# Performance work log

Hardware: AMD Instinct MI355X
Metric: run time of the kernel (lower is better)

The kernel has to match this reference:

```python
import jax, jax.numpy as jnp
import numpy as np

B = 8192          # num_envs
OPT = 16          # num options
SHARED = 22       # shared_state_size (hardcoded in module)
UNIQ = 8          # unique_state_size (hardcoded in module)
MIN_DUR, MAX_DUR = 0.1, 0.5  # const.gait_net.valid_swing_duration_range


def _w(k, o, i):
    return jax.random.normal(k, (o, i), jnp.float32) * (1.0 / np.sqrt(i))


def setup_inputs() -> dict:
    key = jax.random.key(0)
    ks = jax.random.split(key, 20)
    obs = jax.random.normal(ks[0], (B, SHARED + OPT * UNIQ), jnp.float32)
    flag = jax.random.uniform(ks[1], (B, OPT)) < 0.25
    u = obs[:, SHARED:].reshape(B, OPT, UNIQ)
    u = u.at[:, :, 0].set(jnp.where(flag, 1.0, u[:, :, 0]))
    obs = jnp.concatenate([obs[:, :SHARED], u.reshape(B, OPT * UNIQ)], axis=1)
    return {
        "obs": obs,
        "sw1": _w(ks[2], 256, 22), "sb1": jnp.zeros((256,), jnp.float32),
        "sw2": _w(ks[3], 256, 256), "sb2": jnp.zeros((256,), jnp.float32),
        "uw1": _w(ks[4], 128, 8), "ub1": jnp.zeros((128,), jnp.float32),
        "uw2": _w(ks[5], 128, 128), "ub2": jnp.zeros((128,), jnp.float32),
        "no_op_embedding": jax.random.normal(ks[6], (128,), jnp.float32),
        "tw1": _w(ks[7], 512, 384), "tb1": jnp.zeros((512,), jnp.float32),
        "tw2": _w(ks[8], 256, 512), "tb2": jnp.zeros((256,), jnp.float32),
        "vw": _w(ks[9], 1, 256), "vb": jnp.zeros((1,), jnp.float32),
        "dw": _w(ks[10], 1, 256), "db": jnp.zeros((1,), jnp.float32),
    }


def reference(obs, sw1, sb1, sw2, sb2, uw1, ub1, uw2, ub2, no_op_embedding,
              tw1, tb1, tw2, tb2, vw, vb, dw, db):
    relu = jax.nn.relu
    shared = obs[:, :SHARED]                               # [B, 22]
    uniq = obs[:, SHARED:].reshape(B, OPT, UNIQ)           # [B, OPT, 8]
    # shared encoder (22 -> 256 -> 256, relu output)
    se = relu(relu(shared @ sw1.T + sb1) @ sw2.T + sb2)    # [B, 256]
    # unique encoder applied to all options at once (8 -> 128 -> 128)
    ue = relu(relu(uniq @ uw1.T + ub1) @ uw2.T + ub2)      # [B, OPT, 128]
    no_op = uniq[:, :, 0] == 1.0                           # [B, OPT]
    ue = jnp.where(no_op[..., None], no_op_embedding, ue)
    trunk_in = jnp.concatenate(
        [jnp.broadcast_to(se[:, None, :], (B, OPT, se.shape[-1])), ue], axis=-1)
    t = relu(relu(trunk_in @ tw1.T + tb1) @ tw2.T + tb2)   # [B, OPT, 256]
    logits = (t @ vw.T + vb).squeeze(-1)                   # [B, OPT]
    duration = jax.nn.sigmoid((t @ dw.T + db).squeeze(-1)) * (MAX_DUR - MIN_DUR) + MIN_DUR
    return logits, duration
```

## Files before the change

kernel.cpp:

```cpp
#include <hip/hip_runtime.h>
#include <stdint.h>


static constexpr int B_ = 8192;

typedef __attribute__((ext_vector_type(8))) short bf16x8;
typedef __attribute__((ext_vector_type(4))) float f32x4;

__device__ __forceinline__ float u2f(uint16_t u) {
    union { uint32_t i; float f; } c; c.i = (uint32_t)u << 16; return c.f;
}
__device__ __forceinline__ uint16_t f2u(float f) {
    union { float f; uint32_t i; } c; c.f = f;
    uint32_t x = c.i;
    return (uint16_t)((x + 0x7FFFu + ((x >> 16) & 1u)) >> 16);
}

static constexpr size_t WCSE   = 0;
static constexpr size_t WTW1SE = 4194304;
static constexpr size_t WTW1UE = WTW1SE + 131072;
static constexpr size_t WTW2   = WTW1UE + 65536;
static constexpr size_t WUW2   = WTW2 + 131072;
static constexpr size_t WSW2   = WUW2 + 16384;
static constexpr size_t WUW1B  = WSW2 + 65536;

__global__ __launch_bounds__(256) void k_conv(
    const float* __restrict__ tw1, const float* __restrict__ tw2,
    const float* __restrict__ uw2, const float* __restrict__ sw2,
    const float* __restrict__ uw1, uint16_t* __restrict__ ws)
{
    int i4 = blockIdx.x * 256 + threadIdx.x;
    if (i4 >= 102400) {
        int q = i4 - 102400;
        int n = q >> 3, k0 = (q & 7) * 4;
        ushort4 o = {0, 0, 0, 0};
        if (k0 < 8) {
            float4 v = *reinterpret_cast<const float4*>(uw1 + n * 8 + k0);
            o.x = f2u(v.x); o.y = f2u(v.y); o.z = f2u(v.z); o.w = f2u(v.w);
        }
        *reinterpret_cast<ushort4*>(ws + WUW1B + n * 32 + k0) = o;
        return;
    }
    const float* src; size_t dst;
    if (i4 < 32768) {
        int g = i4 * 4, n = g >> 8, k = g & 255;
        src = tw1 + (size_t)n * 384 + k;
        dst = WTW1SE + (size_t)g;
    } else if (i4 < 49152) {
        int q = i4 - 32768, n = q >> 5, w = q & 31;
        src = tw1 + (size_t)n * 384 + 256 + w * 4;
        dst = WTW1UE + (size_t)n * 128 + w * 4;
    } else if (i4 < 81920) {
        int q = (i4 - 49152) * 4;
        src = tw2 + q; dst = WTW2 + q;
    } else if (i4 < 86016) {
        int q = (i4 - 81920) * 4;
        src = uw2 + q; dst = WUW2 + q;
    } else {
        int q = (i4 - 86016) * 4;
        src = sw2 + q; dst = WSW2 + q;
    }
    float4 v = *reinterpret_cast<const float4*>(src);
    ushort4 o;
    o.x = f2u(v.x); o.y = f2u(v.y); o.z = f2u(v.z); o.w = f2u(v.w);
    *reinterpret_cast<ushort4*>(ws + dst) = o;
}

__global__ __launch_bounds__(512) void k_cse(
    const float* __restrict__ obs,
    const float* __restrict__ sw1, const float* __restrict__ sb1,
    const float* __restrict__ sb2, const float* __restrict__ tb1,
    uint16_t* __restrict__ ws)
{
    __shared__ float xs[16][24];
    __shared__ uint16_t h1s[16 * 264];
    __shared__ uint16_t seL[16 * 264];
    const int t = threadIdx.x;
    const int b0 = blockIdx.x * 16;
    const uint16_t* sw2b   = ws + WSW2;
    const uint16_t* tw1seb = ws + WTW1SE;

    if (t < 352) {
        int e = t / 22, c = t - e * 22;
        xs[e][c] = obs[(size_t)(b0 + e) * 150 + c];
    }
    __syncthreads();
    {
        const int n = t & 255;
        float w[22];
        #pragma unroll
        for (int k = 0; k < 22; ++k) w[k] = sw1[n * 22 + k];
        const float bias = sb1[n];
        #pragma unroll
        for (int ii = 0; ii < 8; ++ii) {
            int e = (t >> 8) * 8 + ii;
            float a = bias;
            #pragma unroll
            for (int k = 0; k < 22; ++k) a += w[k] * xs[e][k];
            h1s[e * 264 + n] = f2u(fmaxf(a, 0.f));
        }
    }
    __syncthreads();
    const int wv = t >> 6, lane = t & 63, quad = lane >> 4, l16 = lane & 15;
    {
        f32x4 acc[2];
        #pragma unroll
        for (int nt = 0; nt < 2; ++nt) {
            float bv = sb2[wv * 32 + nt * 16 + l16];
            acc[nt] = {bv, bv, bv, bv};
        }
        const uint16_t* bb = sw2b + (size_t)(wv * 32 + l16) * 256 + quad * 8;
        bf16x8 bc[2], bn[2];
        bc[0] = *reinterpret_cast<const bf16x8*>(bb);
        bc[1] = *reinterpret_cast<const bf16x8*>(bb + 4096);
        #pragma unroll
        for (int kk = 0; kk < 8; ++kk) {
            if (kk < 7) {
                bn[0] = *reinterpret_cast<const bf16x8*>(bb + (kk + 1) * 32);
                bn[1] = *reinterpret_cast<const bf16x8*>(bb + 4096 + (kk + 1) * 32);
            }
            bf16x8 af = *reinterpret_cast<const bf16x8*>(
                &h1s[l16 * 264 + kk * 32 + quad * 8]);
            #pragma unroll
            for (int nt = 0; nt < 2; ++nt)
                acc[nt] = __builtin_amdgcn_mfma_f32_16x16x32_bf16(
                    af, bc[nt], acc[nt], 0, 0, 0);
            bc[0] = bn[0]; bc[1] = bn[1];
        }
        #pragma unroll
        for (int nt = 0; nt < 2; ++nt)
            #pragma unroll
            for (int r = 0; r < 4; ++r)
                seL[(quad * 4 + r) * 264 + wv * 32 + nt * 16 + l16] =
                    f2u(fmaxf(acc[nt][r], 0.f));
    }
    __syncthreads();
    {
        f32x4 acc[4];
        #pragma unroll
        for (int nt = 0; nt < 4; ++nt) {
            float bv = tb1[wv * 64 + nt * 16 + l16];
            acc[nt] = {bv, bv, bv, bv};
        }
        const uint16_t* bb = tw1seb + (size_t)(wv * 64 + l16) * 256 + quad * 8;
        bf16x8 bc[4], bn[4];
        #pragma unroll
        for (int nt = 0; nt < 4; ++nt)
            bc[nt] = *reinterpret_cast<const bf16x8*>(bb + nt * 4096);
        #pragma unroll
        for (int kk = 0; kk < 8; ++kk) {
            if (kk < 7) {
                #pragma unroll
                for (int nt = 0; nt < 4; ++nt)
                    bn[nt] = *reinterpret_cast<const bf16x8*>(
                        bb + nt * 4096 + (kk + 1) * 32);
            }
            bf16x8 af = *reinterpret_cast<const bf16x8*>(
                &seL[l16 * 264 + kk * 32 + quad * 8]);
            #pragma unroll
            for (int nt = 0; nt < 4; ++nt)
                acc[nt] = __builtin_amdgcn_mfma_f32_16x16x32_bf16(
                    af, bc[nt], acc[nt], 0, 0, 0);
            #pragma unroll
            for (int nt = 0; nt < 4; ++nt) bc[nt] = bn[nt];
        }
        #pragma unroll
        for (int nt = 0; nt < 4; ++nt)
            #pragma unroll
            for (int r = 0; r < 4; ++r)
                ws[WCSE + (size_t)(b0 + quad * 4 + r) * 512 +
                   wv * 64 + nt * 16 + l16] = f2u(acc[nt][r]);
    }
}

static constexpr int UQB_OFF  = 0;
static constexpr int NOOP_OFF = 5120;
static constexpr int CSE_OFF  = 5376;
static constexpr int H1U_OFF  = 9472;
static constexpr int UET_OFF  = 26880;
static constexpr int H1T_OFF  = 44288;
static constexpr int SMEM_SZ  = 78080;

__global__ __launch_bounds__(512, 4) void k_main(
    const float* __restrict__ obs,
    const float* __restrict__ ub1,
    const float* __restrict__ ub2, const float* __restrict__ emb,
    const float* __restrict__ tb2,
    const float* __restrict__ vw,  const float* __restrict__ vb,
    const float* __restrict__ dw,  const float* __restrict__ db,
    const uint16_t* __restrict__ wsb,
    float* __restrict__ out)
{
    __shared__ __align__(16) char smem[SMEM_SZ];
    uint16_t* uqb   = (uint16_t*)(smem + UQB_OFF);
    float*    noopf = (float*)(smem + NOOP_OFF);
    uint16_t* cseL  = (uint16_t*)(smem + CSE_OFF);
    uint16_t* h1u   = (uint16_t*)(smem + H1U_OFF);
    uint16_t* uet   = (uint16_t*)(smem + UET_OFF);
    uint16_t* h1t   = (uint16_t*)(smem + H1T_OFF);
    uint16_t* t2    = h1t;

    const int t    = threadIdx.x;
    const int wv   = t >> 6;
    const int lane = t & 63;
    const int quad = lane >> 4;
    const int l16  = lane & 15;
    const int b0   = blockIdx.x * 4;

    const uint16_t* csep  = wsb + WCSE;
    const uint16_t* tw1ue = wsb + WTW1UE;
    const uint16_t* tw2b  = wsb + WTW2;
    const uint16_t* uw2b  = wsb + WUW2;
    const uint16_t* uw1b  = wsb + WUW1B;

    {
        int r = t >> 3, q = t & 7;
        int e = r >> 4, o = r & 15;
        ushort4 ov = {0, 0, 0, 0};
        if (q < 2) {
            const float2* sp = reinterpret_cast<const float2*>(
                &obs[(size_t)(b0 + e) * 150 + 22 + o * 8 + q * 4]);
            float2 a = sp[0], b = sp[1];
            ov.x = f2u(a.x); ov.y = f2u(a.y); ov.z = f2u(b.x); ov.w = f2u(b.y);
        }
        *reinterpret_cast<ushort4*>(&uqb[r * 40 + q * 4]) = ov;
        #pragma unroll
        for (int ii = 0; ii < 2; ++ii) {
            int i = t + ii * 512;
            int ee = i >> 8, cc = i & 255;
            ((uint32_t*)cseL)[ee * 256 + cc] =
                ((const uint32_t*)(csep + (size_t)(b0 + ee) * 512))[cc];
        }
        if (t < 64) {
            int ee = t >> 4, oo = t & 15;
            noopf[t] = (obs[(size_t)(b0 + ee) * 150 + 22 + oo * 8] == 1.0f) ? 1.0f : 0.0f;
        }
    }
    __syncthreads();

    {
        const int n = wv * 16 + l16;
        const float bv = ub1[n];
        f32x4 acc[4];
        #pragma unroll
        for (int mt = 0; mt < 4; ++mt) acc[mt] = {bv, bv, bv, bv};
        bf16x8 bf = *reinterpret_cast<const bf16x8*>(&uw1b[n * 32 + quad * 8]);
        #pragma unroll
        for (int mt = 0; mt < 4; ++mt) {
            bf16x8 af = *reinterpret_cast<const bf16x8*>(
                &uqb[(mt * 16 + l16) * 40 + quad * 8]);
            acc[mt] = __builtin_amdgcn_mfma_f32_16x16x32_bf16(af, bf, acc[mt], 0, 0, 0);
        }
        #pragma unroll
        for (int mt = 0; mt < 4; ++mt)
            #pragma unroll
            for (int r = 0; r < 4; ++r) {
                int row = mt * 16 + quad * 4 + r;
                h1u[row * 136 + n] = f2u(fmaxf(acc[mt][r], 0.f));
            }
    }
    __syncthreads();

    {
        const int n = wv * 16 + l16;
        const float bv = ub2[n];
        const float ev = emb[n];
        f32x4 acc[4];
        #pragma unroll
        for (int mt = 0; mt < 4; ++mt) acc[mt] = {bv, bv, bv, bv};
        #pragma unroll
        for (int kk = 0; kk < 4; ++kk) {
            bf16x8 bf = *reinterpret_cast<const bf16x8*>(
                &uw2b[(size_t)n * 128 + kk * 32 + quad * 8]);
            #pragma unroll
            for (int mt = 0; mt < 4; ++mt) {
                bf16x8 af = *reinterpret_cast<const bf16x8*>(
                    &h1u[(mt * 16 + l16) * 136 + kk * 32 + quad * 8]);
                acc[mt] = __builtin_amdgcn_mfma_f32_16x16x32_bf16(af, bf, acc[mt], 0, 0, 0);
            }
        }
        #pragma unroll
        for (int mt = 0; mt < 4; ++mt)
            #pragma unroll
            for (int r = 0; r < 4; ++r) {
                int row = mt * 16 + quad * 4 + r;
                float v = (noopf[row] != 0.0f) ? ev : fmaxf(acc[mt][r], 0.f);
                uet[row * 136 + n] = f2u(v);
            }
    }
    __syncthreads();

    f32x4 acc2[4][2];
    #pragma unroll
    for (int nt = 0; nt < 2; ++nt) {
        float bv = tb2[wv * 32 + nt * 16 + l16];
        #pragma unroll
        for (int mt = 0; mt < 4; ++mt) acc2[mt][nt] = {bv, bv, bv, bv};
    }

    #pragma unroll
    for (int nc = 0; nc < 2; ++nc) {
        {
            f32x4 acc1[4][2];
            #pragma unroll
            for (int nt = 0; nt < 2; ++nt) {
                int n = nc * 256 + wv * 32 + nt * 16 + l16;
                #pragma unroll
                for (int mt = 0; mt < 4; ++mt) {
                    float v = u2f(cseL[mt * 512 + n]);
                    acc1[mt][nt] = {v, v, v, v};
                }
            }
            const uint16_t* bb = tw1ue + (size_t)(nc * 256 + wv * 32 + l16) * 128
                                 + quad * 8;
            bf16x8 bc[2], bn[2];
            bc[0] = *reinterpret_cast<const bf16x8*>(bb);
            bc[1] = *reinterpret_cast<const bf16x8*>(bb + 2048);
            #pragma unroll
            for (int kk = 0; kk < 4; ++kk) {
                if (kk < 3) {
                    bn[0] = *reinterpret_cast<const bf16x8*>(bb + (kk + 1) * 32);
                    bn[1] = *reinterpret_cast<const bf16x8*>(bb + 2048 + (kk + 1) * 32);
                }
                bf16x8 af[4];
                #pragma unroll
                for (int mt = 0; mt < 4; ++mt)
                    af[mt] = *reinterpret_cast<const bf16x8*>(
                        &uet[(mt * 16 + l16) * 136 + kk * 32 + quad * 8]);
                #pragma unroll
                for (int mt = 0; mt < 4; ++mt)
                    #pragma unroll
                    for (int nt = 0; nt < 2; ++nt)
                        acc1[mt][nt] = __builtin_amdgcn_mfma_f32_16x16x32_bf16(
                            af[mt], bc[nt], acc1[mt][nt], 0, 0, 0);
                bc[0] = bn[0]; bc[1] = bn[1];
            }
            #pragma unroll
            for (int mt = 0; mt < 4; ++mt)
                #pragma unroll
                for (int nt = 0; nt < 2; ++nt)
                    #pragma unroll
                    for (int r = 0; r < 4; ++r) {
                        int row = mt * 16 + quad * 4 + r;
                        h1t[row * 264 + wv * 32 + nt * 16 + l16] =
                            f2u(fmaxf(acc1[mt][nt][r], 0.f));
                    }
        }
        __syncthreads();
        {
            const uint16_t* cb = tw2b + (size_t)(wv * 32 + l16) * 512 + nc * 256
                                 + quad * 8;
            bf16x8 cc[2], cn[2];
            cc[0] = *reinterpret_cast<const bf16x8*>(cb);
            cc[1] = *reinterpret_cast<const bf16x8*>(cb + 8192);
            #pragma unroll
            for (int k2 = 0; k2 < 8; ++k2) {
                if (k2 < 7) {
                    cn[0] = *reinterpret_cast<const bf16x8*>(cb + (k2 + 1) * 32);
                    cn[1] = *reinterpret_cast<const bf16x8*>(cb + 8192 + (k2 + 1) * 32);
                }
                bf16x8 af[4];
                #pragma unroll
                for (int mt = 0; mt < 4; ++mt)
                    af[mt] = *reinterpret_cast<const bf16x8*>(
                        &h1t[(mt * 16 + l16) * 264 + k2 * 32 + quad * 8]);
                #pragma unroll
                for (int mt = 0; mt < 4; ++mt)
                    #pragma unroll
                    for (int nt = 0; nt < 2; ++nt)
                        acc2[mt][nt] = __builtin_amdgcn_mfma_f32_16x16x32_bf16(
                            af[mt], cc[nt], acc2[mt][nt], 0, 0, 0);
                cc[0] = cn[0]; cc[1] = cn[1];
            }
        }
        if (nc == 0) __syncthreads();
    }
    __syncthreads();
    #pragma unroll
    for (int mt = 0; mt < 4; ++mt)
        #pragma unroll
        for (int nt = 0; nt < 2; ++nt)
            #pragma unroll
            for (int r = 0; r < 4; ++r) {
                int row = mt * 16 + quad * 4 + r;
                t2[row * 264 + wv * 32 + nt * 16 + l16] =
                    f2u(fmaxf(acc2[mt][nt][r], 0.f));
            }
    __syncthreads();

    {
        float vwf[4], dwf[4];
        #pragma unroll
        for (int j = 0; j < 4; ++j) {
            vwf[j] = vw[lane + 64 * j];
            dwf[j] = dw[lane + 64 * j];
        }
        const float vbf = vb[0], dbf = db[0];
        #pragma unroll
        for (int rr = 0; rr < 8; ++rr) {
            int row = wv * 8 + rr;
            float sv = 0.f, sd = 0.f;
            #pragma unroll
            for (int j = 0; j < 4; ++j) {
                float tv = u2f(t2[row * 264 + lane + 64 * j]);
                sv += tv * vwf[j];
                sd += tv * dwf[j];
            }
            #pragma unroll
            for (int off = 32; off > 0; off >>= 1) {
                sv += __shfl_down(sv, off);
                sd += __shfl_down(sd, off);
            }
            if (lane == 0) {
                int g = blockIdx.x * 64 + row;
                out[g] = sv + vbf;
                float z = sd + dbf;
                float sig = 1.f / (1.f + __expf(-z));
                out[B_ * 16 + g] = sig * 0.4f + 0.1f;
            }
        }
    }
}

extern "C" void kernel_launch(void* const* d_in, const int* in_sizes, int n_in,
                              void* d_out, int out_size, void* d_ws, size_t ws_size,
                              hipStream_t stream) {
    const float* obs = (const float*)d_in[0];
    const float* sw1 = (const float*)d_in[1];
    const float* sb1 = (const float*)d_in[2];
    const float* sw2 = (const float*)d_in[3];
    const float* sb2 = (const float*)d_in[4];
    const float* uw1 = (const float*)d_in[5];
    const float* ub1 = (const float*)d_in[6];
    const float* uw2 = (const float*)d_in[7];
    const float* ub2 = (const float*)d_in[8];
    const float* emb = (const float*)d_in[9];
    const float* tw1 = (const float*)d_in[10];
    const float* tb1 = (const float*)d_in[11];
    const float* tw2 = (const float*)d_in[12];
    const float* tb2 = (const float*)d_in[13];
    const float* vw  = (const float*)d_in[14];
    const float* vb  = (const float*)d_in[15];
    const float* dw  = (const float*)d_in[16];
    const float* db  = (const float*)d_in[17];

    uint16_t* wsb = (uint16_t*)d_ws;

    k_conv<<<404, 256, 0, stream>>>(tw1, tw2, uw2, sw2, uw1, wsb);
    k_cse<<<512, 512, 0, stream>>>(obs, sw1, sb1, sb2, tb1, wsb);
    k_main<<<B_ / 4, 512, 0, stream>>>(obs, ub1, ub2, emb, tb2,
                                       vw, vb, dw, db, wsb, (float*)d_out);
}
```

Baseline: 238.5 us.

## Merge weight conversion into shared-encoder kernel and read fp32 weights directly

Folds the weight-conversion kernel into the shared-encoder kernel as extra trailing blocks, so one launch goes away. The shared-encoder GEMMs now read sw2 and the shared part of tw1 as fp32 from global memory and convert to bf16 in registers, so those slices no longer need a pre-converted copy. In exchange each block loads twice the bytes for those weights and converts them again, and the software prefetch of B fragments is dropped.

```diff
diff --git a/kernel.cpp b/kernel.cpp
--- a/kernel.cpp
+++ b/kernel.cpp
@@ -15,70 +15,71 @@
     uint32_t x = c.i;
     return (uint16_t)((x + 0x7FFFu + ((x >> 16) & 1u)) >> 16);
 }
+__device__ __forceinline__ bf16x8 cvt8(float4 a, float4 b) {
+    bf16x8 r;
+    r[0] = (short)f2u(a.x); r[1] = (short)f2u(a.y);
+    r[2] = (short)f2u(a.z); r[3] = (short)f2u(a.w);
+    r[4] = (short)f2u(b.x); r[5] = (short)f2u(b.y);
+    r[6] = (short)f2u(b.z); r[7] = (short)f2u(b.w);
+    return r;
+}
 
 static constexpr size_t WCSE   = 0;
-static constexpr size_t WTW1SE = 4194304;
-static constexpr size_t WTW1UE = WTW1SE + 131072;
+static constexpr size_t WTW1UE = 4194304;
 static constexpr size_t WTW2   = WTW1UE + 65536;
 static constexpr size_t WUW2   = WTW2 + 131072;
-static constexpr size_t WSW2   = WUW2 + 16384;
-static constexpr size_t WUW1B  = WSW2 + 65536;
-
-__global__ __launch_bounds__(256) void k_conv(
-    const float* __restrict__ tw1, const float* __restrict__ tw2,
-    const float* __restrict__ uw2, const float* __restrict__ sw2,
-    const float* __restrict__ uw1, uint16_t* __restrict__ ws)
-{
-    int i4 = blockIdx.x * 256 + threadIdx.x;
-    if (i4 >= 102400) {
-        int q = i4 - 102400;
-        int n = q >> 3, k0 = (q & 7) * 4;
-        ushort4 o = {0, 0, 0, 0};
-        if (k0 < 8) {
-            float4 v = *reinterpret_cast<const float4*>(uw1 + n * 8 + k0);
-            o.x = f2u(v.x); o.y = f2u(v.y); o.z = f2u(v.z); o.w = f2u(v.w);
-        }
-        *reinterpret_cast<ushort4*>(ws + WUW1B + n * 32 + k0) = o;
-        return;
-    }
-    const float* src; size_t dst;
-    if (i4 < 32768) {
-        int g = i4 * 4, n = g >> 8, k = g & 255;
-        src = tw1 + (size_t)n * 384 + k;
-        dst = WTW1SE + (size_t)g;
-    } else if (i4 < 49152) {
-        int q = i4 - 32768, n = q >> 5, w = q & 31;
-        src = tw1 + (size_t)n * 384 + 256 + w * 4;
-        dst = WTW1UE + (size_t)n * 128 + w * 4;
-    } else if (i4 < 81920) {
-        int q = (i4 - 49152) * 4;
-        src = tw2 + q; dst = WTW2 + q;
-    } else if (i4 < 86016) {
-        int q = (i4 - 81920) * 4;
-        src = uw2 + q; dst = WUW2 + q;
-    } else {
-        int q = (i4 - 86016) * 4;
-        src = sw2 + q; dst = WSW2 + q;
-    }
-    float4 v = *reinterpret_cast<const float4*>(src);
-    ushort4 o;
-    o.x = f2u(v.x); o.y = f2u(v.y); o.z = f2u(v.z); o.w = f2u(v.w);
-    *reinterpret_cast<ushort4*>(ws + dst) = o;
-}
-
-__global__ __launch_bounds__(512) void k_cse(
+static constexpr size_t WUW1B  = WUW2 + 16384;
+
+__global__ __launch_bounds__(512) void k_front(
     const float* __restrict__ obs,
     const float* __restrict__ sw1, const float* __restrict__ sb1,
-    const float* __restrict__ sb2, const float* __restrict__ tb1,
+    const float* __restrict__ sw2, const float* __restrict__ sb2,
+    const float* __restrict__ uw1,
+    const float* __restrict__ uw2,
+    const float* __restrict__ tw1, const float* __restrict__ tb1,
+    const float* __restrict__ tw2,
     uint16_t* __restrict__ ws)
 {
+    const int t = threadIdx.x;
+
+    if (blockIdx.x >= 512) {
+        int i4 = (blockIdx.x - 512) * 512 + t;
+        if (i4 >= 102400) {
+            int q = i4 - 102400;
+            int n = q >> 3, k0 = (q & 7) * 4;
+            ushort4 o = {0, 0, 0, 0};
+            if (k0 < 8) {
+                float4 v = *reinterpret_cast<const float4*>(uw1 + n * 8 + k0);
+                o.x = f2u(v.x); o.y = f2u(v.y); o.z = f2u(v.z); o.w = f2u(v.w);
+            }
+            *reinterpret_cast<ushort4*>(ws + WUW1B + n * 32 + k0) = o;
+            return;
+        }
+        const float* src; size_t dst;
+        if (i4 < 16384) {
+            int n = i4 >> 5, w = i4 & 31;
+            src = tw1 + (size_t)n * 384 + 256 + w * 4;
+            dst = WTW1UE + (size_t)n * 128 + w * 4;
+        } else if (i4 < 49152) {
+            int q = (i4 - 16384) * 4;
+            src = tw2 + q; dst = WTW2 + q;
+        } else if (i4 < 53248) {
+            int q = (i4 - 49152) * 4;
+            src = uw2 + q; dst = WUW2 + q;
+        } else {
+            return;
+        }
+        float4 v = *reinterpret_cast<const float4*>(src);
+        ushort4 o;
+        o.x = f2u(v.x); o.y = f2u(v.y); o.z = f2u(v.z); o.w = f2u(v.w);
+        *reinterpret_cast<ushort4*>(ws + dst) = o;
+        return;
+    }
+
     __shared__ float xs[16][24];
     __shared__ uint16_t h1s[16 * 264];
     __shared__ uint16_t seL[16 * 264];
-    const int t = threadIdx.x;
     const int b0 = blockIdx.x * 16;
-    const uint16_t* sw2b   = ws + WSW2;
-    const uint16_t* tw1seb = ws + WTW1SE;
 
     if (t < 352) {
         int e = t / 22, c = t - e * 22;
@@ -109,23 +110,19 @@
             float bv = sb2[wv * 32 + nt * 16 + l16];
             acc[nt] = {bv, bv, bv, bv};
         }
-        const uint16_t* bb = sw2b + (size_t)(wv * 32 + l16) * 256 + quad * 8;
-        bf16x8 bc[2], bn[2];
-        bc[0] = *reinterpret_cast<const bf16x8*>(bb);
-        bc[1] = *reinterpret_cast<const bf16x8*>(bb + 4096);
         #pragma unroll
         for (int kk = 0; kk < 8; ++kk) {
-            if (kk < 7) {
-                bn[0] = *reinterpret_cast<const bf16x8*>(bb + (kk + 1) * 32);
-                bn[1] = *reinterpret_cast<const bf16x8*>(bb + 4096 + (kk + 1) * 32);
-            }
             bf16x8 af = *reinterpret_cast<const bf16x8*>(
                 &h1s[l16 * 264 + kk * 32 + quad * 8]);
             #pragma unroll
-            for (int nt = 0; nt < 2; ++nt)
+            for (int nt = 0; nt < 2; ++nt) {
+                const float* wr = sw2 + (size_t)(wv * 32 + nt * 16 + l16) * 256
+                                  + kk * 32 + quad * 8;
+                bf16x8 bf = cvt8(*reinterpret_cast<const float4*>(wr),
+                                 *reinterpret_cast<const float4*>(wr + 4));
                 acc[nt] = __builtin_amdgcn_mfma_f32_16x16x32_bf16(
-                    af, bc[nt], acc[nt], 0, 0, 0);
-            bc[0] = bn[0]; bc[1] = bn[1];
+                    af, bf, acc[nt], 0, 0, 0);
+            }
         }
         #pragma unroll
         for (int nt = 0; nt < 2; ++nt)
@@ -142,27 +139,19 @@
             float bv = tb1[wv * 64 + nt * 16 + l16];
             acc[nt] = {bv, bv, bv, bv};
         }
-        const uint16_t* bb = tw1seb + (size_t)(wv * 64 + l16) * 256 + quad * 8;
-        bf16x8 bc[4], bn[4];
-        #pragma unroll
-        for (int nt = 0; nt < 4; ++nt)
-            bc[nt] = *reinterpret_cast<const bf16x8*>(bb + nt * 4096);
         #pragma unroll
         for (int kk = 0; kk < 8; ++kk) {
-            if (kk < 7) {
-                #pragma unroll
-                for (int nt = 0; nt < 4; ++nt)
-                    bn[nt] = *reinterpret_cast<const bf16x8*>(
-                        bb + nt * 4096 + (kk + 1) * 32);
-            }
             bf16x8 af = *reinterpret_cast<const bf16x8*>(
                 &seL[l16 * 264 + kk * 32 + quad * 8]);
             #pragma unroll
-            for (int nt = 0; nt < 4; ++nt)
+            for (int nt = 0; nt < 4; ++nt) {
+                const float* wr = tw1 + (size_t)(wv * 64 + nt * 16 + l16) * 384
+                                  + kk * 32 + quad * 8;
+                bf16x8 bf = cvt8(*reinterpret_cast<const float4*>(wr),
+                                 *reinterpret_cast<const float4*>(wr + 4));
                 acc[nt] = __builtin_amdgcn_mfma_f32_16x16x32_bf16(
-                    af, bc[nt], acc[nt], 0, 0, 0);
-            #pragma unroll
-            for (int nt = 0; nt < 4; ++nt) bc[nt] = bn[nt];
+                    af, bf, acc[nt], 0, 0, 0);
+            }
         }
         #pragma unroll
         for (int nt = 0; nt < 4; ++nt)
@@ -446,8 +435,8 @@
 
     uint16_t* wsb = (uint16_t*)d_ws;
 
-    k_conv<<<404, 256, 0, stream>>>(tw1, tw2, uw2, sw2, uw1, wsb);
-    k_cse<<<512, 512, 0, stream>>>(obs, sw1, sb1, sb2, tb1, wsb);
+    k_front<<<714, 512, 0, stream>>>(obs, sw1, sb1, sw2, sb2,
+                                     uw1, uw2, tw1, tb1, tw2, wsb);
     k_main<<<B_ / 4, 512, 0, stream>>>(obs, ub1, ub2, emb, tb2,
                                        vw, vb, dw, db, wsb, (float*)d_out);
 }
```

After: 256.8 us. +7.6%, slower.

## Double rows per block in encoder and main kernels with 2D wave tiling

Applied to the files above, without the earlier changes.

k_cse now handles 32 envs per block instead of 16, and k_main handles 8 envs (128 rows) per block instead of 4. Waves in k_main are split into two row halves and four column groups, so each weight fragment loaded from global memory feeds more MFMAs. The trunk hidden layer is now processed in four 128-column chunks with double-buffered LDS, which removes one barrier per chunk. In exchange, LDS use per block grows to about 123KB and launch bounds drop to 2 blocks per CU, which reduces occupancy and halves the grid size.

```diff
diff --git a/kernel.cpp b/kernel.cpp
--- a/kernel.cpp
+++ b/kernel.cpp
@@ -72,16 +72,16 @@
     const float* __restrict__ sb2, const float* __restrict__ tb1,
     uint16_t* __restrict__ ws)
 {
-    __shared__ float xs[16][24];
-    __shared__ uint16_t h1s[16 * 264];
-    __shared__ uint16_t seL[16 * 264];
+    __shared__ float xs[32][24];
+    __shared__ uint16_t h1s[32 * 264];
+    __shared__ uint16_t seL[32 * 264];
     const int t = threadIdx.x;
-    const int b0 = blockIdx.x * 16;
+    const int b0 = blockIdx.x * 32;
     const uint16_t* sw2b   = ws + WSW2;
     const uint16_t* tw1seb = ws + WTW1SE;
 
-    if (t < 352) {
-        int e = t / 22, c = t - e * 22;
+    for (int i = t; i < 704; i += 512) {
+        int e = i / 22, c = i - e * 22;
         xs[e][c] = obs[(size_t)(b0 + e) * 150 + c];
     }
     __syncthreads();
@@ -92,8 +92,8 @@
         for (int k = 0; k < 22; ++k) w[k] = sw1[n * 22 + k];
         const float bias = sb1[n];
         #pragma unroll
-        for (int ii = 0; ii < 8; ++ii) {
-            int e = (t >> 8) * 8 + ii;
+        for (int ii = 0; ii < 16; ++ii) {
+            int e = (t >> 8) * 16 + ii;
             float a = bias;
             #pragma unroll
             for (int k = 0; k < 22; ++k) a += w[k] * xs[e][k];
@@ -103,11 +103,12 @@
     __syncthreads();
     const int wv = t >> 6, lane = t & 63, quad = lane >> 4, l16 = lane & 15;
     {
-        f32x4 acc[2];
+        f32x4 acc[2][2];
         #pragma unroll
         for (int nt = 0; nt < 2; ++nt) {
             float bv = sb2[wv * 32 + nt * 16 + l16];
-            acc[nt] = {bv, bv, bv, bv};
+            acc[0][nt] = {bv, bv, bv, bv};
+            acc[1][nt] = {bv, bv, bv, bv};
         }
         const uint16_t* bb = sw2b + (size_t)(wv * 32 + l16) * 256 + quad * 8;
         bf16x8 bc[2], bn[2];
@@ -119,28 +120,36 @@
                 bn[0] = *reinterpret_cast<const bf16x8*>(bb + (kk + 1) * 32);
                 bn[1] = *reinterpret_cast<const bf16x8*>(bb + 4096 + (kk + 1) * 32);
             }
-            bf16x8 af = *reinterpret_cast<const bf16x8*>(
-                &h1s[l16 * 264 + kk * 32 + quad * 8]);
+            bf16x8 af[2];
+            #pragma unroll
+            for (int mt = 0; mt < 2; ++mt)
+                af[mt] = *reinterpret_cast<const bf16x8*>(
+                    &h1s[(mt * 16 + l16) * 264 + kk * 32 + quad * 8]);
+            #pragma unroll
+            for (int mt = 0; mt < 2; ++mt)
+                #pragma unroll
+                for (int nt = 0; nt < 2; ++nt)
+                    acc[mt][nt] = __builtin_amdgcn_mfma_f32_16x16x32_bf16(
+                        af[mt], bc[nt], acc[mt][nt], 0, 0, 0);
+            bc[0] = bn[0]; bc[1] = bn[1];
+        }
+        #pragma unroll
+        for (int mt = 0; mt < 2; ++mt)
             #pragma unroll
             for (int nt = 0; nt < 2; ++nt)
-                acc[nt] = __builtin_amdgcn_mfma_f32_16x16x32_bf16(
-                    af, bc[nt], acc[nt], 0, 0, 0);
-            bc[0] = bn[0]; bc[1] = bn[1];
-        }
-        #pragma unroll
-        for (int nt = 0; nt < 2; ++nt)
-            #pragma unroll
-            for (int r = 0; r < 4; ++r)
-                seL[(quad * 4 + r) * 264 + wv * 32 + nt * 16 + l16] =
-                    f2u(fmaxf(acc[nt][r], 0.f));
-    }
-    __syncthreads();
-    {
-        f32x4 acc[4];
+                #pragma unroll
+                for (int r = 0; r < 4; ++r)
+                    seL[(mt * 16 + quad * 4 + r) * 264 + wv * 32 + nt * 16 + l16] =
+                        f2u(fmaxf(acc[mt][nt][r], 0.f));
+    }
+    __syncthreads();
+    {
+        f32x4 acc[2][4];
         #pragma unroll
         for (int nt = 0; nt < 4; ++nt) {
             float bv = tb1[wv * 64 + nt * 16 + l16];
-            acc[nt] = {bv, bv, bv, bv};
+            acc[0][nt] = {bv, bv, bv, bv};
+            acc[1][nt] = {bv, bv, bv, bv};
         }
         const uint16_t* bb = tw1seb + (size_t)(wv * 64 + l16) * 256 + quad * 8;
         bf16x8 bc[4], bn[4];
@@ -155,33 +164,40 @@
                     bn[nt] = *reinterpret_cast<const bf16x8*>(
                         bb + nt * 4096 + (kk + 1) * 32);
             }
-            bf16x8 af = *reinterpret_cast<const bf16x8*>(
-                &seL[l16 * 264 + kk * 32 + quad * 8]);
+            bf16x8 af[2];
+            #pragma unroll
+            for (int mt = 0; mt < 2; ++mt)
+                af[mt] = *reinterpret_cast<const bf16x8*>(
+                    &seL[(mt * 16 + l16) * 264 + kk * 32 + quad * 8]);
+            #pragma unroll
+            for (int mt = 0; mt < 2; ++mt)
+                #pragma unroll
+                for (int nt = 0; nt < 4; ++nt)
+                    acc[mt][nt] = __builtin_amdgcn_mfma_f32_16x16x32_bf16(
+                        af[mt], bc[nt], acc[mt][nt], 0, 0, 0);
+            #pragma unroll
+            for (int nt = 0; nt < 4; ++nt) bc[nt] = bn[nt];
+        }
+        #pragma unroll
+        for (int mt = 0; mt < 2; ++mt)
             #pragma unroll
             for (int nt = 0; nt < 4; ++nt)
-                acc[nt] = __builtin_amdgcn_mfma_f32_16x16x32_bf16(
-                    af, bc[nt], acc[nt], 0, 0, 0);
-            #pragma unroll
-            for (int nt = 0; nt < 4; ++nt) bc[nt] = bn[nt];
-        }
-        #pragma unroll
-        for (int nt = 0; nt < 4; ++nt)
-            #pragma unroll
-            for (int r = 0; r < 4; ++r)
-                ws[WCSE + (size_t)(b0 + quad * 4 + r) * 512 +
-                   wv * 64 + nt * 16 + l16] = f2u(acc[nt][r]);
+                #pragma unroll
+                for (int r = 0; r < 4; ++r)
+                    ws[WCSE + (size_t)(b0 + mt * 16 + quad * 4 + r) * 512 +
+                       wv * 64 + nt * 16 + l16] = f2u(acc[mt][nt][r]);
     }
 }
 
 static constexpr int UQB_OFF  = 0;
-static constexpr int NOOP_OFF = 5120;
-static constexpr int CSE_OFF  = 5376;
-static constexpr int H1U_OFF  = 9472;
-static constexpr int UET_OFF  = 26880;
-static constexpr int H1T_OFF  = 44288;
-static constexpr int SMEM_SZ  = 78080;
-
-__global__ __launch_bounds__(512, 4) void k_main(
+static constexpr int NOOP_OFF = 10240;
+static constexpr int CSE_OFF  = 10752;
+static constexpr int UET_OFF  = 18944;
+static constexpr int H1TA_OFF = 53760;
+static constexpr int H1TB_OFF = 88576;
+static constexpr int SMEM_SZ  = 123392;
+
+__global__ __launch_bounds__(512, 2) void k_main(
     const float* __restrict__ obs,
     const float* __restrict__ ub1,
     const float* __restrict__ ub2, const float* __restrict__ emb,
@@ -195,17 +211,20 @@
     uint16_t* uqb   = (uint16_t*)(smem + UQB_OFF);
     float*    noopf = (float*)(smem + NOOP_OFF);
     uint16_t* cseL  = (uint16_t*)(smem + CSE_OFF);
-    uint16_t* h1u   = (uint16_t*)(smem + H1U_OFF);
     uint16_t* uet   = (uint16_t*)(smem + UET_OFF);
-    uint16_t* h1t   = (uint16_t*)(smem + H1T_OFF);
-    uint16_t* t2    = h1t;
+    uint16_t* h1ta  = (uint16_t*)(smem + H1TA_OFF);
+    uint16_t* h1tb  = (uint16_t*)(smem + H1TB_OFF);
+    uint16_t* h1u   = h1ta;
+    uint16_t* t2    = uet;
 
     const int t    = threadIdx.x;
     const int wv   = t >> 6;
     const int lane = t & 63;
     const int quad = lane >> 4;
     const int l16  = lane & 15;
-    const int b0   = blockIdx.x * 4;
+    const int mh   = wv >> 2;
+    const int ng   = wv & 3;
+    const int b0   = blockIdx.x * 8;
 
     const uint16_t* csep  = wsb + WCSE;
     const uint16_t* tw1ue = wsb + WTW1UE;
@@ -214,24 +233,28 @@
     const uint16_t* uw1b  = wsb + WUW1B;
 
     {
-        int r = t >> 3, q = t & 7;
-        int e = r >> 4, o = r & 15;
-        ushort4 ov = {0, 0, 0, 0};
-        if (q < 2) {
-            const float2* sp = reinterpret_cast<const float2*>(
-                &obs[(size_t)(b0 + e) * 150 + 22 + o * 8 + q * 4]);
-            float2 a = sp[0], b = sp[1];
-            ov.x = f2u(a.x); ov.y = f2u(a.y); ov.z = f2u(b.x); ov.w = f2u(b.y);
-        }
-        *reinterpret_cast<ushort4*>(&uqb[r * 40 + q * 4]) = ov;
         #pragma unroll
         for (int ii = 0; ii < 2; ++ii) {
+            int idx = t + ii * 512;
+            int r = idx >> 3, q = idx & 7;
+            int e = r >> 4, o = r & 15;
+            ushort4 ov = {0, 0, 0, 0};
+            if (q < 2) {
+                const float2* sp = reinterpret_cast<const float2*>(
+                    &obs[(size_t)(b0 + e) * 150 + 22 + o * 8 + q * 4]);
+                float2 a = sp[0], b = sp[1];
+                ov.x = f2u(a.x); ov.y = f2u(a.y); ov.z = f2u(b.x); ov.w = f2u(b.y);
+            }
+            *reinterpret_cast<ushort4*>(&uqb[r * 40 + q * 4]) = ov;
+        }
+        #pragma unroll
+        for (int ii = 0; ii < 4; ++ii) {
             int i = t + ii * 512;
             int ee = i >> 8, cc = i & 255;
             ((uint32_t*)cseL)[ee * 256 + cc] =
                 ((const uint32_t*)(csep + (size_t)(b0 + ee) * 512))[cc];
         }
-        if (t < 64) {
+        if (t < 128) {
             int ee = t >> 4, oo = t & 15;
             noopf[t] = (obs[(size_t)(b0 + ee) * 150 + 22 + oo * 8] == 1.0f) ? 1.0f : 0.0f;
         }
@@ -239,80 +262,111 @@
     __syncthreads();
 
     {
-        const int n = wv * 16 + l16;
-        const float bv = ub1[n];
-        f32x4 acc[4];
-        #pragma unroll
-        for (int mt = 0; mt < 4; ++mt) acc[mt] = {bv, bv, bv, bv};
-        bf16x8 bf = *reinterpret_cast<const bf16x8*>(&uw1b[n * 32 + quad * 8]);
+        f32x4 acc[4][2];
+        #pragma unroll
+        for (int nt = 0; nt < 2; ++nt) {
+            float bv = ub1[ng * 32 + nt * 16 + l16];
+            #pragma unroll
+            for (int mt = 0; mt < 4; ++mt) acc[mt][nt] = {bv, bv, bv, bv};
+        }
+        bf16x8 bf[2];
+        #pragma unroll
+        for (int nt = 0; nt < 2; ++nt)
+            bf[nt] = *reinterpret_cast<const bf16x8*>(
+                &uw1b[(ng * 32 + nt * 16 + l16) * 32 + quad * 8]);
         #pragma unroll
         for (int mt = 0; mt < 4; ++mt) {
             bf16x8 af = *reinterpret_cast<const bf16x8*>(
-                &uqb[(mt * 16 + l16) * 40 + quad * 8]);
-            acc[mt] = __builtin_amdgcn_mfma_f32_16x16x32_bf16(af, bf, acc[mt], 0, 0, 0);
+                &uqb[(mh * 64 + mt * 16 + l16) * 40 + quad * 8]);
+            #pragma unroll
+            for (int nt = 0; nt < 2; ++nt)
+                acc[mt][nt] = __builtin_amdgcn_mfma_f32_16x16x32_bf16(
+                    af, bf[nt], acc[mt][nt], 0, 0, 0);
         }
         #pragma unroll
         for (int mt = 0; mt < 4; ++mt)
             #pragma unroll
-            for (int r = 0; r < 4; ++r) {
-                int row = mt * 16 + quad * 4 + r;
-                h1u[row * 136 + n] = f2u(fmaxf(acc[mt][r], 0.f));
-            }
-    }
-    __syncthreads();
-
-    {
-        const int n = wv * 16 + l16;
-        const float bv = ub2[n];
-        const float ev = emb[n];
-        f32x4 acc[4];
-        #pragma unroll
-        for (int mt = 0; mt < 4; ++mt) acc[mt] = {bv, bv, bv, bv};
+            for (int nt = 0; nt < 2; ++nt)
+                #pragma unroll
+                for (int r = 0; r < 4; ++r) {
+                    int row = mh * 64 + mt * 16 + quad * 4 + r;
+                    h1u[row * 136 + ng * 32 + nt * 16 + l16] =
+                        f2u(fmaxf(acc[mt][nt][r], 0.f));
+                }
+    }
+    __syncthreads();
+
+    {
+        f32x4 acc[4][2];
+        float ev[2];
+        #pragma unroll
+        for (int nt = 0; nt < 2; ++nt) {
+            int n = ng * 32 + nt * 16 + l16;
+            float bv = ub2[n];
+            ev[nt] = emb[n];
+            #pragma unroll
+            for (int mt = 0; mt < 4; ++mt) acc[mt][nt] = {bv, bv, bv, bv};
+        }
+        const uint16_t* bb = uw2b + (size_t)(ng * 32 + l16) * 128 + quad * 8;
+        bf16x8 bc[2], bn[2];
+        bc[0] = *reinterpret_cast<const bf16x8*>(bb);
+        bc[1] = *reinterpret_cast<const bf16x8*>(bb + 2048);
         #pragma unroll
         for (int kk = 0; kk < 4; ++kk) {
-            bf16x8 bf = *reinterpret_cast<const bf16x8*>(
-                &uw2b[(size_t)n * 128 + kk * 32 + quad * 8]);
-            #pragma unroll
-            for (int mt = 0; mt < 4; ++mt) {
-                bf16x8 af = *reinterpret_cast<const bf16x8*>(
-                    &h1u[(mt * 16 + l16) * 136 + kk * 32 + quad * 8]);
-                acc[mt] = __builtin_amdgcn_mfma_f32_16x16x32_bf16(af, bf, acc[mt], 0, 0, 0);
-            }
-        }
+            if (kk < 3) {
+                bn[0] = *reinterpret_cast<const bf16x8*>(bb + (kk + 1) * 32);
+                bn[1] = *reinterpret_cast<const bf16x8*>(bb + 2048 + (kk + 1) * 32);
+            }
+            bf16x8 af[4];
+            #pragma unroll
+            for (int mt = 0; mt < 4; ++mt)
+                af[mt] = *reinterpret_cast<const bf16x8*>(
+                    &h1u[(mh * 64 + mt * 16 + l16) * 136 + kk * 32 + quad * 8]);
+            #pragma unroll
+            for (int mt = 0; mt < 4; ++mt)
+                #pragma unroll
+                for (int nt = 0; nt < 2; ++nt)
+                    acc[mt][nt] = __builtin_amdgcn_mfma_f32_16x16x32_bf16(
+                        af[mt], bc[nt], acc[mt][nt], 0, 0, 0);
+            bc[0] = bn[0]; bc[1] = bn[1];
+        }
+        __syncthreads();
         #pragma unroll
         for (int mt = 0; mt < 4; ++mt)
             #pragma unroll
-            for (int r = 0; r < 4; ++r) {
-                int row = mt * 16 + quad * 4 + r;
-                float v = (noopf[row] != 0.0f) ? ev : fmaxf(acc[mt][r], 0.f);
-                uet[row * 136 + n] = f2u(v);
-            }
-    }
-    __syncthreads();
-
-    f32x4 acc2[4][2];
+            for (int nt = 0; nt < 2; ++nt)
+                #pragma unroll
+                for (int r = 0; r < 4; ++r) {
+                    int row = mh * 64 + mt * 16 + quad * 4 + r;
+                    float v = (noopf[row] != 0.0f) ? ev[nt] : fmaxf(acc[mt][nt][r], 0.f);
+                    uet[row * 136 + ng * 32 + nt * 16 + l16] = f2u(v);
+                }
+    }
+    __syncthreads();
+
+    f32x4 acc2[4][4];
     #pragma unroll
-    for (int nt = 0; nt < 2; ++nt) {
-        float bv = tb2[wv * 32 + nt * 16 + l16];
+    for (int nt = 0; nt < 4; ++nt) {
+        float bv = tb2[ng * 64 + nt * 16 + l16];
         #pragma unroll
         for (int mt = 0; mt < 4; ++mt) acc2[mt][nt] = {bv, bv, bv, bv};
     }
 
-    #pragma unroll
-    for (int nc = 0; nc < 2; ++nc) {
+    for (int nc = 0; nc < 4; ++nc) {
+        uint16_t* hw = (nc & 1) ? h1tb : h1ta;
         {
             f32x4 acc1[4][2];
             #pragma unroll
             for (int nt = 0; nt < 2; ++nt) {
-                int n = nc * 256 + wv * 32 + nt * 16 + l16;
+                int n = nc * 128 + ng * 32 + nt * 16 + l16;
                 #pragma unroll
                 for (int mt = 0; mt < 4; ++mt) {
-                    float v = u2f(cseL[mt * 512 + n]);
+                    float v = u2f(cseL[(mh * 4 + mt) * 512 + n]);
                     acc1[mt][nt] = {v, v, v, v};
                 }
             }
-            const uint16_t* bb = tw1ue + (size_t)(nc * 256 + wv * 32 + l16) * 128
-                                 + quad * 8;
+            const uint16_t* bb = tw1ue +
+                (size_t)(nc * 128 + ng * 32 + l16) * 128 + quad * 8;
             bf16x8 bc[2], bn[2];
             bc[0] = *reinterpret_cast<const bf16x8*>(bb);
             bc[1] = *reinterpret_cast<const bf16x8*>(bb + 2048);
@@ -326,7 +380,7 @@
                 #pragma unroll
                 for (int mt = 0; mt < 4; ++mt)
                     af[mt] = *reinterpret_cast<const bf16x8*>(
-                        &uet[(mt * 16 + l16) * 136 + kk * 32 + quad * 8]);
+                        &uet[(mh * 64 + mt * 16 + l16) * 136 + kk * 32 + quad * 8]);
                 #pragma unroll
                 for (int mt = 0; mt < 4; ++mt)
                     #pragma unroll
@@ -341,49 +395,52 @@
                 for (int nt = 0; nt < 2; ++nt)
                     #pragma unroll
                     for (int r = 0; r < 4; ++r) {
-                        int row = mt * 16 + quad * 4 + r;
-                        h1t[row * 264 + wv * 32 + nt * 16 + l16] =
+                        int row = mh * 64 + mt * 16 + quad * 4 + r;
+                        hw[row * 136 + ng * 32 + nt * 16 + l16] =
                             f2u(fmaxf(acc1[mt][nt][r], 0.f));
                     }
         }
         __syncthreads();
         {
-            const uint16_t* cb = tw2b + (size_t)(wv * 32 + l16) * 512 + nc * 256
-                                 + quad * 8;
-            bf16x8 cc[2], cn[2];
-            cc[0] = *reinterpret_cast<const bf16x8*>(cb);
-            cc[1] = *reinterpret_cast<const bf16x8*>(cb + 8192);
-            #pragma unroll
-            for (int k2 = 0; k2 < 8; ++k2) {
-                if (k2 < 7) {
-                    cn[0] = *reinterpret_cast<const bf16x8*>(cb + (k2 + 1) * 32);
-                    cn[1] = *reinterpret_cast<const bf16x8*>(cb + 8192 + (k2 + 1) * 32);
+            const uint16_t* cb = tw2b + (size_t)(ng * 64 + l16) * 512 +
+                                 nc * 128 + quad * 8;
+            bf16x8 cc[4], cn[4];
+            #pragma unroll
+            for (int nt = 0; nt < 4; ++nt)
+                cc[nt] = *reinterpret_cast<const bf16x8*>(cb + nt * 8192);
+            #pragma unroll
+            for (int k2 = 0; k2 < 4; ++k2) {
+                if (k2 < 3) {
+                    #pragma unroll
+                    for (int nt = 0; nt < 4; ++nt)
+                        cn[nt] = *reinterpret_cast<const bf16x8*>(
+                            cb + nt * 8192 + (k2 + 1) * 32);
                 }
                 bf16x8 af[4];
                 #pragma unroll
                 for (int mt = 0; mt < 4; ++mt)
                     af[mt] = *reinterpret_cast<const bf16x8*>(
-                        &h1t[(mt * 16 + l16) * 264 + k2 * 32 + quad * 8]);
+                        &hw[(mh * 64 + mt * 16 + l16) * 136 + k2 * 32 + quad * 8]);
                 #pragma unroll
                 for (int mt = 0; mt < 4; ++mt)
                     #pragma unroll
-                    for (int nt = 0; nt < 2; ++nt)
+                    for (int nt = 0; nt < 4; ++nt)
                         acc2[mt][nt] = __builtin_amdgcn_mfma_f32_16x16x32_bf16(
                             af[mt], cc[nt], acc2[mt][nt], 0, 0, 0);
-                cc[0] = cn[0]; cc[1] = cn[1];
-            }
-        }
-        if (nc == 0) __syncthreads();
+                #pragma unroll
+                for (int nt = 0; nt < 4; ++nt) cc[nt] = cn[nt];
+            }
+        }
     }
     __syncthreads();
     #pragma unroll
     for (int mt = 0; mt < 4; ++mt)
         #pragma unroll
-        for (int nt = 0; nt < 2; ++nt)
+        for (int nt = 0; nt < 4; ++nt)
             #pragma unroll
             for (int r = 0; r < 4; ++r) {
-                int row = mt * 16 + quad * 4 + r;
-                t2[row * 264 + wv * 32 + nt * 16 + l16] =
+                int row = mh * 64 + mt * 16 + quad * 4 + r;
+                t2[row * 264 + ng * 64 + nt * 16 + l16] =
                     f2u(fmaxf(acc2[mt][nt][r], 0.f));
             }
     __syncthreads();
@@ -397,8 +454,8 @@
         }
         const float vbf = vb[0], dbf = db[0];
         #pragma unroll
-        for (int rr = 0; rr < 8; ++rr) {
-            int row = wv * 8 + rr;
+        for (int rr = 0; rr < 16; ++rr) {
+            int row = wv * 16 + rr;
             float sv = 0.f, sd = 0.f;
             #pragma unroll
             for (int j = 0; j < 4; ++j) {
@@ -412,7 +469,7 @@
                 sd += __shfl_down(sd, off);
             }
             if (lane == 0) {
-                int g = blockIdx.x * 64 + row;
+                int g = blockIdx.x * 128 + row;
                 out[g] = sv + vbf;
                 float z = sd + dbf;
                 float sig = 1.f / (1.f + __expf(-z));
@@ -447,7 +504,7 @@
     uint16_t* wsb = (uint16_t*)d_ws;
 
     k_conv<<<404, 256, 0, stream>>>(tw1, tw2, uw2, sw2, uw1, wsb);
-    k_cse<<<512, 512, 0, stream>>>(obs, sw1, sb1, sb2, tb1, wsb);
-    k_main<<<B_ / 4, 512, 0, stream>>>(obs, ub1, ub2, emb, tb2,
+    k_cse<<<256, 512, 0, stream>>>(obs, sw1, sb1, sb2, tb1, wsb);
+    k_main<<<B_ / 8, 512, 0, stream>>>(obs, ub1, ub2, emb, tb2,
                                        vw, vb, dw, db, wsb, (float*)d_out);
 }
```

Result: slower. 254.6 us (+6.7%).
